# Kernel tuning notes

Measured on AMD Instinct MI355X. Metric: run time of the kernel, lower is better.

The kernel has to match this reference:

```python
import jax, jax.numpy as jnp
from jax import lax
import numpy as np

EMBED = 20
FILTERS = 16
KSIZES = (1, 3, 5, 7, 9)
LIN_IN = 7 * len(KSIZES) * FILTERS  # 560
LIN_DIM = 64
SEQ_LENS = {'pep': 12, 'a1': 7, 'a2': 8, 'a3': 16, 'b1': 6, 'b2': 7, 'b3': 18}
BATCH = 16384


def setup_inputs() -> dict:
    key = jax.random.key(0)
    keys = jax.random.split(key, 16)
    inp = {}
    for i, (name, L) in enumerate(SEQ_LENS.items()):
        inp[name] = jax.random.normal(keys[i], (BATCH, EMBED, L), dtype=jnp.float32)
    # Conv weights: one stacked array per kernel size, [7 sequences, FILTERS, EMBED, k]
    for j, k in enumerate(KSIZES):
        inp[f'Wk{k}'] = jax.random.normal(keys[7 + j], (7, FILTERS, EMBED, k), dtype=jnp.float32) * 0.1
    inp['lin1_w'] = jax.random.normal(keys[12], (LIN_DIM, LIN_IN), dtype=jnp.float32) * 0.05
    inp['lin1_b'] = jnp.zeros((LIN_DIM,), dtype=jnp.float32)
    inp['lin2_w'] = jax.random.normal(keys[13], (1, LIN_DIM), dtype=jnp.float32) * 0.1
    inp['lin2_b'] = jnp.zeros((1,), dtype=jnp.float32)
    return inp


def _conv_relu_gmax(x, w):
    # x: [B, C, L], w: [F, C, k] -> SAME conv + ReLU + global max over length -> [B, F]
    y = lax.conv_general_dilated(x, w, window_strides=(1,), padding='SAME',
                                 dimension_numbers=('NCH', 'OIH', 'NCH'))
    return jnp.max(jax.nn.relu(y), axis=-1)


def _branch(x, ws):
    # x scaled by 1/5 as in the torch forward; concat pooled features over kernel sizes
    x = x / 5.0
    return jnp.concatenate([_conv_relu_gmax(x, w) for w in ws], axis=1)  # [B, 5*F]


def reference(pep, a1, a2, a3, b1, b2, b3, Wk1, Wk3, Wk5, Wk7, Wk9,
              lin1_w, lin1_b, lin2_w, lin2_b):
    seqs = [pep, a1, a2, a3, b1, b2, b3]
    Wks = [Wk1, Wk3, Wk5, Wk7, Wk9]
    feats = jnp.concatenate(
        [_branch(seqs[i], [W[i] for W in Wks]) for i in range(7)], axis=1)  # [B, 560]
    # Dropout is identity at inference.
    h = jax.nn.sigmoid(feats @ lin1_w.T + lin1_b)  # [B, 64]
    out = h @ lin2_w.T + lin2_b                    # [B, 1]
    return out.reshape(-1)                          # [B]
```

## Files before the change

kernel.cpp:

```cpp
#include <hip/hip_runtime.h>
#include <stdint.h>
#include <stddef.h>

typedef short bfrag __attribute__((ext_vector_type(8)));
typedef float f32x4 __attribute__((ext_vector_type(4)));

#define NSEQ 7

__constant__ int c_ks[5] = {1, 3, 5, 7, 9};

#define SLO0 3
#define SLO1 2
#define SLO2 1
#define SLO3 0
#define SLO4 0
#define SN0 1
#define SN1 3
#define SN2 5
#define SN3 6
#define SN4 7

#define STAGE_MAX_HW 10368
#define XL_HW (STAGE_MAX_HW + 2560)

static __device__ __forceinline__ unsigned short f2bf(float f) {
  unsigned int u = __float_as_uint(f);
  u += 0x7FFFu + ((u >> 16) & 1u);
  return (unsigned short)(u >> 16);
}

struct PrepArgs {
  const float* Wk[5];
  const float* lin1_w;
  bfrag* Wpack;
  bfrag* lin1pack;
};

__global__ __launch_bounds__(256) void prep_kernel(PrepArgs a) {
  int tid = blockIdx.x * 256 + threadIdx.x;
  const int NW = NSEQ * 5 * 7 * 64;
  if (tid < NW) {
    int lane = tid & 63, rest = tid >> 6;
    int step = rest % 7, nt = (rest / 7) % 5, seq = rest / 35;
    int quad = lane >> 4, f = lane & 15;
    int ks = c_ks[nt], off = (9 - ks) >> 1;
    const float* W = a.Wk[nt];
    bfrag s;
#pragma unroll
    for (int j = 0; j < 8; ++j) {
      int k = step * 32 + quad * 8 + j;
      int t = k / 24, c = k % 24;
      int tap = t - off;
      float val = 0.f;
      if (c < 20 && tap >= 0 && tap < ks)
        val = W[((seq * 16 + f) * 20 + c) * ks + tap] * 0.2f;
      s[j] = (short)f2bf(val);
    }
    a.Wpack[tid] = s;
  } else if (tid < NW + 4 * 18 * 64) {
    int t2 = tid - NW;
    int lane = t2 & 63, rest = t2 >> 6;
    int step = rest % 18, nt = rest / 18;
    int quad = lane >> 4, col = lane & 15;
    int n = nt * 16 + col;
    bfrag s;
#pragma unroll
    for (int j = 0; j < 8; ++j) {
      int k = step * 32 + quad * 8 + j;
      float val = (k < 560) ? a.lin1_w[n * 560 + k] : 0.f;
      s[j] = (short)f2bf(val);
    }
    a.lin1pack[t2] = s;
  }
}

struct ConvArgs {
  const float* x[NSEQ];
  const bfrag* Wpack;
  unsigned short* feats;
};

template <int SLO, int SN>
static __device__ __forceinline__ void mfma_group(f32x4& acc, int s, const bfrag& Af,
                                                  const bfrag* BfBase) {
  if (s >= SLO && s < SLO + SN)
    acc = __builtin_amdgcn_mfma_f32_16x16x32_bf16(Af, BfBase[s - SLO], acc, 0, 0, 0);
}

static __device__ __forceinline__ void tile_mfma(const unsigned short* arow, const bfrag* Bf,
                                                 f32x4 acc[5]) {
#pragma unroll
  for (int s = 0; s < 7; ++s) {
    bfrag Af = *(const bfrag*)(arow + s * 32);
    mfma_group<SLO0, SN0>(acc[0], s, Af, Bf + 0);
    mfma_group<SLO1, SN1>(acc[1], s, Af, Bf + 1);
    mfma_group<SLO2, SN2>(acc[2], s, Af, Bf + 4);
    mfma_group<SLO3, SN3>(acc[3], s, Af, Bf + 9);
    acc[4] = __builtin_amdgcn_mfma_f32_16x16x32_bf16(Af, Bf[15 + s], acc[4], 0, 0, 0);
  }
}

template <int L>
__device__ __forceinline__ void conv_body(unsigned short* xl, const ConvArgs& a,
                                          const int seq, const int b0) {
  constexpr int Pv = L + 9;
  constexpr int SHW = Pv * 24;
  constexpr int STAGE_HW = 16 * SHW;
  int* pmax = (int*)(xl + STAGE_MAX_HW);
  const int tid = threadIdx.x;
  const float* xg = a.x[seq];

  for (int i = tid; i < STAGE_HW / 8; i += 256) ((uint4*)xl)[i] = uint4{0, 0, 0, 0};
  for (int i = tid; i < 320; i += 256) ((uint4*)pmax)[i] = uint4{0, 0, 0, 0};
  __syncthreads();
  for (int r = tid; r < 16 * 20; r += 256) {
    int b = r / 20, c = r % 20;
    const float* src = xg + ((size_t)(b0 + b) * 20 + c) * L;
    unsigned short* dst = xl + b * SHW + 4 * 24 + c;
#pragma unroll
    for (int xi = 0; xi < L; ++xi) dst[xi * 24] = f2bf(src[xi]);
  }
  __syncthreads();

  const int wave = tid >> 6, lane = tid & 63, quad = lane >> 4, m = lane & 15;

  const bfrag* wp = a.Wpack + (size_t)(seq * 5 * 7) * 64 + lane;
  bfrag Bf[22];
  {
    int bi = 0;
#pragma unroll
    for (int i = 0; i < SN0; ++i) Bf[bi++] = wp[(0 * 7 + SLO0 + i) * 64];
#pragma unroll
    for (int i = 0; i < SN1; ++i) Bf[bi++] = wp[(1 * 7 + SLO1 + i) * 64];
#pragma unroll
    for (int i = 0; i < SN2; ++i) Bf[bi++] = wp[(2 * 7 + SLO2 + i) * 64];
#pragma unroll
    for (int i = 0; i < SN3; ++i) Bf[bi++] = wp[(3 * 7 + SLO3 + i) * 64];
#pragma unroll
    for (int i = 0; i < SN4; ++i) Bf[bi++] = wp[(4 * 7 + SLO4 + i) * 64];
  }

  for (int tile = wave; tile < L; tile += 4) {
    int r = tile * 16 + m;
    int bl = r / L;
    int l = r - bl * L;
    const unsigned short* arow = &xl[bl * SHW + l * 24 + quad * 8];
    f32x4 acc[5];
#pragma unroll
    for (int g = 0; g < 5; ++g) acc[g] = f32x4{0.f, 0.f, 0.f, 0.f};
    tile_mfma(arow, Bf, acc);

    int r0 = tile * 16 + quad * 4;
    int s0 = r0 / L;
    int l0 = r0 - s0 * L;
    int base0 = s0 * 80 + m;
#pragma unroll
    for (int g = 0; g < 5; ++g) {
      float v0 = fmaxf(acc[g][0], 0.f);
      float v1 = fmaxf(acc[g][1], 0.f);
      float v2 = fmaxf(acc[g][2], 0.f);
      float v3 = fmaxf(acc[g][3], 0.f);
      if constexpr ((L & 3) == 0) {
        float va = fmaxf(fmaxf(v0, v1), fmaxf(v2, v3));
        atomicMax(&pmax[base0 + g * 16], __float_as_int(va));
      } else {
        int cnt = L - l0;
        float a1 = cnt > 1 ? v1 : 0.f, b1_ = cnt > 1 ? 0.f : v1;
        float a2 = cnt > 2 ? v2 : 0.f, b2_ = cnt > 2 ? 0.f : v2;
        float a3 = cnt > 3 ? v3 : 0.f, b3_ = cnt > 3 ? 0.f : v3;
        float va = fmaxf(fmaxf(v0, a1), fmaxf(a2, a3));
        atomicMax(&pmax[base0 + g * 16], __float_as_int(va));
        if (cnt < 4) {
          float vb = fmaxf(b1_, fmaxf(b2_, b3_));
          atomicMax(&pmax[base0 + 80 + g * 16], __float_as_int(vb));
        }
      }
    }
  }
  __syncthreads();

  if (tid < 160) {
    int s = tid / 10, c = tid - (tid / 10) * 10;
    int k0 = seq * 80 + c * 8;
    bfrag outv;
#pragma unroll
    for (int j = 0; j < 8; ++j)
      outv[j] = (short)f2bf(__int_as_float(pmax[s * 80 + c * 8 + j]));
    int step = k0 >> 5, q = (k0 >> 3) & 3;
    int b = b0 + s;
    *(bfrag*)(a.feats + ((size_t)(b >> 4) * 18 + step) * 512 + (size_t)(q * 16 + (b & 15)) * 8) = outv;
  }
}

__global__ __launch_bounds__(256, 4) void conv_kernel(ConvArgs a) {
  __shared__ __align__(16) unsigned short xl[XL_HW];
  const int bid = blockIdx.x;
  const int seq = bid % 7;
  const int b0 = (bid / 7) * 16;
  switch (seq) {
    case 0: conv_body<12>(xl, a, 0, b0); break;
    case 1: conv_body< 7>(xl, a, 1, b0); break;
    case 2: conv_body< 8>(xl, a, 2, b0); break;
    case 3: conv_body<16>(xl, a, 3, b0); break;
    case 4: conv_body< 6>(xl, a, 4, b0); break;
    case 5: conv_body< 7>(xl, a, 5, b0); break;
    default: conv_body<18>(xl, a, 6, b0); break;
  }
}

struct MlpArgs {
  const bfrag* feats;
  const bfrag* lin1pack;
  const float* lin1_b;
  const float* lin2_w;
  const float* lin2_b;
  float* out;
};

__global__ __launch_bounds__(256, 4) void mlp_kernel(MlpArgs a) {
  __shared__ float h[16 * 68];
  __shared__ float w2[64];
  const int tid = threadIdx.x;
  const int b0 = blockIdx.x * 16;
  if (tid < 64) w2[tid] = a.lin2_w[tid];
  const int wave = tid >> 6, lane = tid & 63, quad = lane >> 4, m = lane & 15;
  const int nt = wave;
  bfrag Bf[18];
#pragma unroll
  for (int s = 0; s < 18; ++s) Bf[s] = a.lin1pack[(nt * 18 + s) * 64 + lane];
  const bfrag* ap = a.feats + (size_t)blockIdx.x * 18 * 64 + lane;
  f32x4 acc = {0.f, 0.f, 0.f, 0.f};
#pragma unroll
  for (int s = 0; s < 18; ++s)
    acc = __builtin_amdgcn_mfma_f32_16x16x32_bf16(ap[s * 64], Bf[s], acc, 0, 0, 0);
  int n = nt * 16 + m;
  float bias = a.lin1_b[n];
#pragma unroll
  for (int r = 0; r < 4; ++r) {
    float pre = acc[r] + bias;
    h[(quad * 4 + r) * 68 + n] = 1.f / (1.f + __expf(-pre));
  }
  __syncthreads();
  int bl = tid >> 4, q = tid & 15;
  const float* hr = &h[bl * 68 + q * 4];
  float s = hr[0] * w2[q * 4] + hr[1] * w2[q * 4 + 1] + hr[2] * w2[q * 4 + 2] + hr[3] * w2[q * 4 + 3];
  s += __shfl_xor(s, 1);
  s += __shfl_xor(s, 2);
  s += __shfl_xor(s, 4);
  s += __shfl_xor(s, 8);
  if (q == 0) a.out[b0 + bl] = s + a.lin2_b[0];
}

extern "C" void kernel_launch(void* const* d_in, const int* in_sizes, int n_in,
                              void* d_out, int out_size, void* d_ws, size_t ws_size,
                              hipStream_t stream) {
  (void)in_sizes; (void)n_in; (void)out_size; (void)ws_size;
  char* ws = (char*)d_ws;
  bfrag* Wpack = (bfrag*)(ws + 0);
  bfrag* lin1pack = (bfrag*)(ws + 262144);
  unsigned short* feats = (unsigned short*)(ws + 393216);

  PrepArgs pa;
  for (int j = 0; j < 5; ++j) pa.Wk[j] = (const float*)d_in[7 + j];
  pa.lin1_w = (const float*)d_in[12];
  pa.Wpack = Wpack;
  pa.lin1pack = lin1pack;
  prep_kernel<<<80, 256, 0, stream>>>(pa);

  ConvArgs ca;
  for (int i = 0; i < NSEQ; ++i) ca.x[i] = (const float*)d_in[i];
  ca.Wpack = Wpack;
  ca.feats = feats;
  conv_kernel<<<7168, 256, 0, stream>>>(ca);

  MlpArgs ma;
  ma.feats = (const bfrag*)feats;
  ma.lin1pack = lin1pack;
  ma.lin1_b = (const float*)d_in[13];
  ma.lin2_w = (const float*)d_in[14];
  ma.lin2_b = (const float*)d_in[15];
  ma.out = (float*)d_out;
  mlp_kernel<<<1024, 256, 0, stream>>>(ma);
}
```

Before: 182.2 us.

## Map MFMA rows to batch per position, pad LDS stride, pack bf16 staging

Each MFMA tile now covers 16 batch samples at one sequence position instead of a flattened batch×length row range. This removes the div/mod row mapping and the split-boundary masking. The max is kept in registers across positions and written with one set of LDS atomicMax per wave at the end, instead of atomics after every tile. The per-sample LDS stride is padded so that rows from different samples fall on different banks, which enlarges the staging area. Input staging converts two channels at once with v_cvt_pk_bf16_f32 and 32-bit LDS stores, but only 160 of the 256 threads take part.

```diff
diff --git a/kernel.cpp b/kernel.cpp
--- a/kernel.cpp
+++ b/kernel.cpp
@@ -20,7 +20,7 @@
 #define SN3 6
 #define SN4 7
 
-#define STAGE_MAX_HW 10368
+#define STAGE_MAX_HW 10624
 #define XL_HW (STAGE_MAX_HW + 2560)
 
 static __device__ __forceinline__ unsigned short f2bf(float f) {
@@ -104,7 +104,8 @@
 __device__ __forceinline__ void conv_body(unsigned short* xl, const ConvArgs& a,
                                           const int seq, const int b0) {
   constexpr int Pv = L + 9;
-  constexpr int SHW = Pv * 24;
+  constexpr int SHW0 = Pv * 24;
+  constexpr int SHW = SHW0 + ((24 - (SHW0 & 63)) & 63);
   constexpr int STAGE_HW = 16 * SHW;
   int* pmax = (int*)(xl + STAGE_MAX_HW);
   const int tid = threadIdx.x;
@@ -113,12 +114,17 @@
   for (int i = tid; i < STAGE_HW / 8; i += 256) ((uint4*)xl)[i] = uint4{0, 0, 0, 0};
   for (int i = tid; i < 320; i += 256) ((uint4*)pmax)[i] = uint4{0, 0, 0, 0};
   __syncthreads();
-  for (int r = tid; r < 16 * 20; r += 256) {
-    int b = r / 20, c = r % 20;
-    const float* src = xg + ((size_t)(b0 + b) * 20 + c) * L;
-    unsigned short* dst = xl + b * SHW + 4 * 24 + c;
-#pragma unroll
-    for (int xi = 0; xi < L; ++xi) dst[xi * 24] = f2bf(src[xi]);
+  for (int r = tid; r < 160; r += 256) {
+    int b = r / 10, cp = r - (r / 10) * 10;
+    const float* s0 = xg + ((size_t)(b0 + b) * 20 + 2 * cp) * L;
+    unsigned short* dst = xl + b * SHW + 4 * 24 + 2 * cp;
+#pragma unroll
+    for (int xi = 0; xi < L; ++xi) {
+      float lo = s0[xi], hi = s0[xi + L];
+      unsigned int pk;
+      asm("v_cvt_pk_bf16_f32 %0, %1, %2" : "=v"(pk) : "v"(lo), "v"(hi));
+      *(unsigned int*)(dst + xi * 24) = pk;
+    }
   }
   __syncthreads();
 
@@ -140,42 +146,28 @@
     for (int i = 0; i < SN4; ++i) Bf[bi++] = wp[(4 * 7 + SLO4 + i) * 64];
   }
 
-  for (int tile = wave; tile < L; tile += 4) {
-    int r = tile * 16 + m;
-    int bl = r / L;
-    int l = r - bl * L;
-    const unsigned short* arow = &xl[bl * SHW + l * 24 + quad * 8];
+  f32x4 vmax[5];
+#pragma unroll
+  for (int g = 0; g < 5; ++g) vmax[g] = f32x4{0.f, 0.f, 0.f, 0.f};
+
+  for (int l = wave; l < L; l += 4) {
+    const unsigned short* arow = &xl[m * SHW + l * 24 + quad * 8];
     f32x4 acc[5];
 #pragma unroll
     for (int g = 0; g < 5; ++g) acc[g] = f32x4{0.f, 0.f, 0.f, 0.f};
     tile_mfma(arow, Bf, acc);
-
-    int r0 = tile * 16 + quad * 4;
-    int s0 = r0 / L;
-    int l0 = r0 - s0 * L;
-    int base0 = s0 * 80 + m;
 #pragma unroll
     for (int g = 0; g < 5; ++g) {
-      float v0 = fmaxf(acc[g][0], 0.f);
-      float v1 = fmaxf(acc[g][1], 0.f);
-      float v2 = fmaxf(acc[g][2], 0.f);
-      float v3 = fmaxf(acc[g][3], 0.f);
-      if constexpr ((L & 3) == 0) {
-        float va = fmaxf(fmaxf(v0, v1), fmaxf(v2, v3));
-        atomicMax(&pmax[base0 + g * 16], __float_as_int(va));
-      } else {
-        int cnt = L - l0;
-        float a1 = cnt > 1 ? v1 : 0.f, b1_ = cnt > 1 ? 0.f : v1;
-        float a2 = cnt > 2 ? v2 : 0.f, b2_ = cnt > 2 ? 0.f : v2;
-        float a3 = cnt > 3 ? v3 : 0.f, b3_ = cnt > 3 ? 0.f : v3;
-        float va = fmaxf(fmaxf(v0, a1), fmaxf(a2, a3));
-        atomicMax(&pmax[base0 + g * 16], __float_as_int(va));
-        if (cnt < 4) {
-          float vb = fmaxf(b1_, fmaxf(b2_, b3_));
-          atomicMax(&pmax[base0 + 80 + g * 16], __float_as_int(vb));
-        }
-      }
-    }
+#pragma unroll
+      for (int r4 = 0; r4 < 4; ++r4) vmax[g][r4] = fmaxf(vmax[g][r4], acc[g][r4]);
+    }
+  }
+
+#pragma unroll
+  for (int g = 0; g < 5; ++g) {
+#pragma unroll
+    for (int r4 = 0; r4 < 4; ++r4)
+      atomicMax(&pmax[(quad * 4 + r4) * 80 + g * 16 + m], __float_as_int(vmax[g][r4]));
   }
   __syncthreads();
 
```

Result: slower. 227.3 us (+24.8%).
